# Optimization experiments

Measured on AMD Instinct MI355X. Metric: run time of the kernel, lower is better.

Reference implementation:

```python
import jax, jax.numpy as jnp
import numpy as np

N = 50000
E = 800000
D_IN = 128
HID = 128
LAT = 64
NEG_SLOPE = 0.2


def setup_inputs() -> dict:
    key = jax.random.key(0)
    ks = jax.random.split(key, 16)
    g = lambda k, shape: jax.random.normal(k, shape, dtype=jnp.float32) * (1.0 / np.sqrt(shape[0]))
    x = jax.random.normal(ks[0], (N, D_IN), dtype=jnp.float32)
    edge_index = jax.random.randint(ks[1], (2, E), 0, N, dtype=jnp.int64)
    return {
        "x": x,
        "edge_index": edge_index,
        # lin1: Linear(D_IN, HID)
        "lin1_w": g(ks[2], (D_IN, HID)),
        "lin1_b": jnp.zeros((HID,), jnp.float32),
        # conv1: GATConv((D_IN, D_IN) -> HID), heads=1
        "w1_src": g(ks[3], (D_IN, HID)),
        "w1_dst": g(ks[4], (D_IN, HID)),
        "a1_src": g(ks[5], (HID,)),
        "a1_dst": g(ks[6], (HID,)),
        "b1": jnp.zeros((HID,), jnp.float32),
        # conv2: GATConv((HID, HID) -> LAT), heads=1
        "w2_src": g(ks[7], (HID, LAT)),
        "w2_dst": g(ks[8], (HID, LAT)),
        "a2_src": g(ks[9], (LAT,)),
        "a2_dst": g(ks[10], (LAT,)),
        "b2": jnp.zeros((LAT,), jnp.float32),
    }


def _gat_conv(x, src, dst, w_src, w_dst, a_src, a_dst, b):
    """PyG GATConv, heads=1, add_self_loops=False. x: [N, Din]."""
    n = x.shape[0]
    hs = x @ w_src                    # [N, C] messages (source transform)
    hd = x @ w_dst                    # [N, C] destination transform
    alpha_s = hs @ a_src              # [N]
    alpha_d = hd @ a_dst              # [N]
    e = jax.nn.leaky_relu(alpha_s[src] + alpha_d[dst], NEG_SLOPE)  # [E]
    # segment softmax over incoming edges per destination node
    m = jax.ops.segment_max(e, dst, num_segments=n)
    ex = jnp.exp(e - m[dst])
    denom = jax.ops.segment_sum(ex, dst, num_segments=n)
    alpha = ex / (denom[dst] + 1e-16)                              # [E]
    msg = hs[src] * alpha[:, None]                                 # [E, C]
    out = jax.ops.segment_sum(msg, dst, num_segments=n)            # [N, C]
    return out + b


def reference(x, edge_index, lin1_w, lin1_b, w1_src, w1_dst, a1_src, a1_dst, b1,
              w2_src, w2_dst, a2_src, a2_dst, b2):
    src, dst = edge_index[0], edge_index[1]
    z = _gat_conv(x, src, dst, w1_src, w1_dst, a1_src, a1_dst, b1)
    z = jax.nn.relu(z + x @ lin1_w + lin1_b)
    z = _gat_conv(z, src, dst, w2_src, w2_dst, a2_src, a2_dst, b2)
    return z
```

## Files before the change

kernel.cpp:

```cpp
#include <hip/hip_runtime.h>

static constexpr int N_NODES = 50000;
static constexpr int N_EDGES = 800000;
static constexpr int NPART = 8;
static constexpr int PART_SZ = N_NODES / NPART;
static constexpr int NTILES = N_NODES / 16;

typedef __attribute__((ext_vector_type(8))) short bf16x8;
typedef __attribute__((ext_vector_type(4))) float f32x4;

__device__ __forceinline__ float bf2f(unsigned short u) {
  union { unsigned int i; float f; } v; v.i = ((unsigned int)u) << 16; return v.f;
}
__device__ __forceinline__ unsigned short f2bf(float f) {
  union { unsigned int i; float f; } v; v.f = f;
  unsigned int r = (v.i + 0x7fffu + ((v.i >> 16) & 1u)) >> 16;
  return (unsigned short)r;
}
__device__ __forceinline__ int clampN(int v) {
  unsigned u = (unsigned)v; return (u < (unsigned)N_NODES) ? (int)u : 0;
}

__global__ void k_zero_out(float* __restrict__ out, int n) {
  int i = blockIdx.x * 256 + threadIdx.x;
  if (i < n) out[i] = 0.f;
}

__global__ void k_zero_da(int* __restrict__ deg, float* __restrict__ as1) {
  int i = blockIdx.x * 256 + threadIdx.x;
  if (i < N_NODES) { deg[i] = 0; as1[i] = 0.f; }
}

__global__ void k_compact(const int* __restrict__ ei,
                          int* __restrict__ s32, int* __restrict__ d32) {
  int e = blockIdx.x * 256 + threadIdx.x;
  if (e < N_EDGES) {
    int z = ei[1] | ei[3] | ei[5] | ei[7];
    int f = (z == 0) ? 1 : 0;
    s32[e] = clampN(ei[(size_t)e << f]);
    d32[e] = clampN(ei[(size_t)(N_EDGES + e) << f]);
  }
}

__global__ void k_prepw(const float* __restrict__ w1_src, const float* __restrict__ wlin,
                        const float* __restrict__ w2_src,
                        const float* __restrict__ w1_dst, const float* __restrict__ a1_dst,
                        const float* __restrict__ w2_dst, const float* __restrict__ a2_dst,
                        unsigned short* __restrict__ w1T, unsigned short* __restrict__ w2T,
                        float* __restrict__ c1dst, float* __restrict__ c2dst) {
  int idx = blockIdx.x * 256 + threadIdx.x;
  if (idx < 256 * 128) {
    int c = idx >> 7, k = idx & 127;
    float v = (c < 128) ? w1_src[k * 128 + c] : wlin[k * 128 + (c - 128)];
    w1T[idx] = f2bf(v);
  } else if (idx < 256 * 128 + 64 * 128) {
    int r = idx - 256 * 128;
    int c = r >> 7, k = r & 127;
    w2T[r] = f2bf(w2_src[k * 64 + c]);
  } else if (blockIdx.x == 160) {
    int k = threadIdx.x;
    if (k < 128) {
      float s1 = 0.f;
      for (int c = 0; c < 128; ++c) s1 += w1_dst[k * 128 + c] * a1_dst[c];
      c1dst[k] = s1;
      float s2 = 0.f;
      for (int c = 0; c < 64; ++c) s2 += w2_dst[k * 64 + c] * a2_dst[c];
      c2dst[k] = s2;
    }
  }
}

__global__ __launch_bounds__(256) void k_prepx(
    const float* __restrict__ x, const float* __restrict__ c1dst,
    unsigned short* __restrict__ xb, float* __restrict__ ad1) {
  int gid = blockIdx.x * 256 + threadIdx.x;
  int row = gid >> 4, sl = gid & 15;
  const float* p = x + (size_t)row * 128 + sl * 8;
  float4 a0 = *(const float4*)p;
  float4 a1 = *(const float4*)(p + 4);
  uint4 o;
  o.x = (unsigned)f2bf(a0.x) | ((unsigned)f2bf(a0.y) << 16);
  o.y = (unsigned)f2bf(a0.z) | ((unsigned)f2bf(a0.w) << 16);
  o.z = (unsigned)f2bf(a1.x) | ((unsigned)f2bf(a1.y) << 16);
  o.w = (unsigned)f2bf(a1.z) | ((unsigned)f2bf(a1.w) << 16);
  *(uint4*)(xb + (size_t)row * 128 + sl * 8) = o;
  float4 ca = *(const float4*)(c1dst + sl * 8);
  float4 cb = *(const float4*)(c1dst + sl * 8 + 4);
  float sd = a0.x * ca.x + a0.y * ca.y + a0.z * ca.z + a0.w * ca.w +
             a1.x * cb.x + a1.y * cb.y + a1.z * cb.z + a1.w * cb.w;
  sd += __shfl_xor(sd, 1, 64);
  sd += __shfl_xor(sd, 2, 64);
  sd += __shfl_xor(sd, 4, 64);
  sd += __shfl_xor(sd, 8, 64);
  if (sl == 0) ad1[row] = sd;
}

__global__ __launch_bounds__(256) void k_gemm1(
    const unsigned short* __restrict__ xb, const unsigned short* __restrict__ w1T,
    const float* __restrict__ lin_b, const float* __restrict__ a1_src,
    unsigned short* __restrict__ hs1, unsigned short* __restrict__ linzb,
    float* __restrict__ as1) {
  int tid = threadIdx.x;
  int wv = tid >> 6, l = tid & 63;
  int lrow = l & 15, lk = l >> 4;
  int cb = wv * 64;
  bf16x8 wfrag[4][4];
#pragma unroll
  for (int ct = 0; ct < 4; ++ct)
#pragma unroll
    for (int ks = 0; ks < 4; ++ks)
      wfrag[ct][ks] = *(const bf16x8*)(w1T + (size_t)(cb + ct * 16 + lrow) * 128 + ks * 32 + lk * 8);
  for (int t = blockIdx.x; t < NTILES; t += gridDim.x) {
    int row = t * 16 + lrow;
    bf16x8 xfrag[4];
#pragma unroll
    for (int ks = 0; ks < 4; ++ks)
      xfrag[ks] = *(const bf16x8*)(xb + (size_t)row * 128 + ks * 32 + lk * 8);
    f32x4 acc[4] = {{0.f,0.f,0.f,0.f},{0.f,0.f,0.f,0.f},{0.f,0.f,0.f,0.f},{0.f,0.f,0.f,0.f}};
#pragma unroll
    for (int ks = 0; ks < 4; ++ks)
#pragma unroll
      for (int ct = 0; ct < 4; ++ct)
        acc[ct] = __builtin_amdgcn_mfma_f32_16x16x32_bf16(wfrag[ct][ks], xfrag[ks], acc[ct], 0, 0, 0);
    if (cb < 128) {
      float pa = 0.f;
#pragma unroll
      for (int ct = 0; ct < 4; ++ct) {
        int col0 = cb + ct * 16 + lk * 4;
        float4 av = *(const float4*)(a1_src + col0);
        pa += acc[ct][0] * av.x + acc[ct][1] * av.y + acc[ct][2] * av.z + acc[ct][3] * av.w;
        uint2 pv;
        pv.x = (unsigned)f2bf(acc[ct][0]) | ((unsigned)f2bf(acc[ct][1]) << 16);
        pv.y = (unsigned)f2bf(acc[ct][2]) | ((unsigned)f2bf(acc[ct][3]) << 16);
        *(uint2*)(hs1 + (size_t)row * 128 + col0) = pv;
      }
      pa += __shfl_xor(pa, 16, 64);
      pa += __shfl_xor(pa, 32, 64);
      if (l < 16) atomicAdd(&as1[t * 16 + l], pa);
    } else {
#pragma unroll
      for (int ct = 0; ct < 4; ++ct) {
        int col0 = cb - 128 + ct * 16 + lk * 4;
        float4 bv = *(const float4*)(lin_b + col0);
        uint2 pv;
        pv.x = (unsigned)f2bf(acc[ct][0] + bv.x) | ((unsigned)f2bf(acc[ct][1] + bv.y) << 16);
        pv.y = (unsigned)f2bf(acc[ct][2] + bv.z) | ((unsigned)f2bf(acc[ct][3] + bv.w) << 16);
        *(uint2*)(linzb + (size_t)row * 128 + col0) = pv;
      }
    }
  }
}

__global__ __launch_bounds__(256) void k_gemm2(
    const unsigned short* __restrict__ zb, const unsigned short* __restrict__ w2T,
    const float* __restrict__ a2_src, const float* __restrict__ c2dst,
    unsigned short* __restrict__ hs2, float* __restrict__ as2, float* __restrict__ ad2) {
  int tid = threadIdx.x;
  int wv = tid >> 6, l = tid & 63;
  int lrow = l & 15, lk = l >> 4;
  int g = blockIdx.x * 4 + wv;
  if (g >= NTILES) return;
  bf16x8 wfrag[4][4];
#pragma unroll
  for (int ct = 0; ct < 4; ++ct)
#pragma unroll
    for (int ks = 0; ks < 4; ++ks)
      wfrag[ct][ks] = *(const bf16x8*)(w2T + (size_t)(ct * 16 + lrow) * 128 + ks * 32 + lk * 8);
  int row = g * 16 + lrow;
  bf16x8 xfrag[4];
  float sd = 0.f;
#pragma unroll
  for (int ks = 0; ks < 4; ++ks) {
    bf16x8 af = *(const bf16x8*)(zb + (size_t)row * 128 + ks * 32 + lk * 8);
    xfrag[ks] = af;
    int k0 = ks * 32 + lk * 8;
    float4 ca = *(const float4*)(c2dst + k0);
    float4 cb = *(const float4*)(c2dst + k0 + 4);
    sd += bf2f((unsigned short)af[0]) * ca.x + bf2f((unsigned short)af[1]) * ca.y +
          bf2f((unsigned short)af[2]) * ca.z + bf2f((unsigned short)af[3]) * ca.w +
          bf2f((unsigned short)af[4]) * cb.x + bf2f((unsigned short)af[5]) * cb.y +
          bf2f((unsigned short)af[6]) * cb.z + bf2f((unsigned short)af[7]) * cb.w;
  }
  sd += __shfl_xor(sd, 16, 64);
  sd += __shfl_xor(sd, 32, 64);
  if (lk == 0) ad2[row] = sd;

  f32x4 acc[4] = {{0.f,0.f,0.f,0.f},{0.f,0.f,0.f,0.f},{0.f,0.f,0.f,0.f},{0.f,0.f,0.f,0.f}};
#pragma unroll
  for (int ks = 0; ks < 4; ++ks)
#pragma unroll
    for (int ct = 0; ct < 4; ++ct)
      acc[ct] = __builtin_amdgcn_mfma_f32_16x16x32_bf16(wfrag[ct][ks], xfrag[ks], acc[ct], 0, 0, 0);
  float pa = 0.f;
#pragma unroll
  for (int ct = 0; ct < 4; ++ct) {
    int col0 = ct * 16 + lk * 4;
    float4 av = *(const float4*)(a2_src + col0);
    pa += acc[ct][0] * av.x + acc[ct][1] * av.y + acc[ct][2] * av.z + acc[ct][3] * av.w;
    uint2 pv;
    pv.x = (unsigned)f2bf(acc[ct][0]) | ((unsigned)f2bf(acc[ct][1]) << 16);
    pv.y = (unsigned)f2bf(acc[ct][2]) | ((unsigned)f2bf(acc[ct][3]) << 16);
    *(uint2*)(hs2 + (size_t)row * 64 + col0) = pv;
  }
  pa += __shfl_xor(pa, 16, 64);
  pa += __shfl_xor(pa, 32, 64);
  if (lk == 0) as2[row] = pa;
}

__global__ void k_count(const int* __restrict__ d32, int* __restrict__ deg) {
  int part = blockIdx.x & (NPART - 1);
  int e = (blockIdx.x >> 3) * 256 + threadIdx.x;
  if (e < N_EDGES) {
    int d = d32[e];
    int lo = part * PART_SZ;
    if (d >= lo && d < lo + PART_SZ) atomicAdd(&deg[d], 1);
  }
}

__global__ __launch_bounds__(256) void k_scan1(const int* __restrict__ deg,
                                               int* __restrict__ offs,
                                               int* __restrict__ bsums, int n) {
  __shared__ int wsum[4];
  int i = blockIdx.x * 256 + threadIdx.x;
  int lane = threadIdx.x & 63, wid = threadIdx.x >> 6;
  int v = (i < n) ? deg[i] : 0;
  int s = v;
#pragma unroll
  for (int o = 1; o < 64; o <<= 1) { int t = __shfl_up(s, o, 64); if (lane >= o) s += t; }
  if (lane == 63) wsum[wid] = s;
  __syncthreads();
  if (threadIdx.x == 0) {
    int a = 0;
#pragma unroll
    for (int w = 0; w < 4; ++w) { a += wsum[w]; wsum[w] = a; }
  }
  __syncthreads();
  int base = (wid > 0) ? wsum[wid - 1] : 0;
  if (i < n) offs[i] = base + s - v;
  if (threadIdx.x == 0) bsums[blockIdx.x] = wsum[3];
}

__global__ __launch_bounds__(256) void k_scan2(int* __restrict__ bsums, int nb,
                                               int* __restrict__ offs, int n, int etot) {
  __shared__ int wsum[4];
  int tid = threadIdx.x, lane = tid & 63, wid = tid >> 6;
  int v = (tid < nb) ? bsums[tid] : 0;
  int s = v;
#pragma unroll
  for (int o = 1; o < 64; o <<= 1) { int t = __shfl_up(s, o, 64); if (lane >= o) s += t; }
  if (lane == 63) wsum[wid] = s;
  __syncthreads();
  if (tid == 0) {
    int a = 0;
#pragma unroll
    for (int w = 0; w < 4; ++w) { a += wsum[w]; wsum[w] = a; }
  }
  __syncthreads();
  int base = (wid > 0) ? wsum[wid - 1] : 0;
  if (tid < nb) bsums[tid] = base + s - v;
  if (tid == 0) offs[n] = etot;
}

__global__ __launch_bounds__(256) void k_scan3(int* __restrict__ offs, int* __restrict__ cursor,
                                               const int* __restrict__ bsums, int n) {
  int i = blockIdx.x * 256 + threadIdx.x;
  if (i < n) {
    int o = offs[i] + bsums[blockIdx.x];
    offs[i] = o;
    cursor[i] = o;
  }
}

__global__ void k_fill(const int* __restrict__ s32, const int* __restrict__ d32,
                       int* __restrict__ cursor, int* __restrict__ ssrc) {
  int part = blockIdx.x & (NPART - 1);
  int e = (blockIdx.x >> 3) * 256 + threadIdx.x;
  if (e < N_EDGES) {
    int d = d32[e];
    int lo = part * PART_SZ;
    if (d >= lo && d < lo + PART_SZ) {
      int p = atomicAdd(&cursor[d], 1);
      if ((unsigned)p < (unsigned)N_EDGES) ssrc[p] = s32[e];
    }
  }
}

__global__ __launch_bounds__(256) void k_agg1(
    const int* __restrict__ offs, const int* __restrict__ ssrc,
    const float* __restrict__ as_, const float* __restrict__ ad_,
    const unsigned short* __restrict__ hs1, const float* __restrict__ b1,
    unsigned short* __restrict__ linzb) {
  int node = (int)((blockIdx.x * 256 + threadIdx.x) >> 6);
  if (node >= N_NODES) return;
  int lane = threadIdx.x & 63;
  int g = lane >> 4, cl = lane & 15;
  int o0 = offs[node], o1 = offs[node + 1];
  if (!((unsigned)o0 <= (unsigned)N_EDGES && (unsigned)o1 <= (unsigned)N_EDGES && o0 <= o1))
    { o0 = 0; o1 = 0; }
  int deg = o1 - o0;
  float ad = ad_[node];
  float acc[8];
#pragma unroll
  for (int k = 0; k < 8; ++k) acc[k] = 0.f;
  float ssum = 0.f;
  for (int j = g; j < deg; j += 4) {
    int s = clampN(ssrc[o0 + j]);
    float e = as_[s] + ad;
    e = e > 0.f ? e : 0.2f * e;
    float w = __expf(e);
    uint4 hv = *(const uint4*)(hs1 + (size_t)s * 128 + cl * 8);
    ssum += w;
    acc[0] += w * __uint_as_float(hv.x << 16);
    acc[1] += w * __uint_as_float(hv.x & 0xffff0000u);
    acc[2] += w * __uint_as_float(hv.y << 16);
    acc[3] += w * __uint_as_float(hv.y & 0xffff0000u);
    acc[4] += w * __uint_as_float(hv.z << 16);
    acc[5] += w * __uint_as_float(hv.z & 0xffff0000u);
    acc[6] += w * __uint_as_float(hv.w << 16);
    acc[7] += w * __uint_as_float(hv.w & 0xffff0000u);
  }
  ssum += __shfl_xor(ssum, 16, 64);
  ssum += __shfl_xor(ssum, 32, 64);
#pragma unroll
  for (int k = 0; k < 8; ++k) {
    acc[k] += __shfl_xor(acc[k], 16, 64);
    acc[k] += __shfl_xor(acc[k], 32, 64);
  }
  if (g == 0) {
    float inv = 1.f / (ssum + 1e-16f);
    uint4 lv = *(const uint4*)(linzb + (size_t)node * 128 + cl * 8);
    float4 ba = *(const float4*)(b1 + cl * 8);
    float4 bb = *(const float4*)(b1 + cl * 8 + 4);
    float z[8];
    z[0] = acc[0] * inv + ba.x + __uint_as_float(lv.x << 16);
    z[1] = acc[1] * inv + ba.y + __uint_as_float(lv.x & 0xffff0000u);
    z[2] = acc[2] * inv + ba.z + __uint_as_float(lv.y << 16);
    z[3] = acc[3] * inv + ba.w + __uint_as_float(lv.y & 0xffff0000u);
    z[4] = acc[4] * inv + bb.x + __uint_as_float(lv.z << 16);
    z[5] = acc[5] * inv + bb.y + __uint_as_float(lv.z & 0xffff0000u);
    z[6] = acc[6] * inv + bb.z + __uint_as_float(lv.w << 16);
    z[7] = acc[7] * inv + bb.w + __uint_as_float(lv.w & 0xffff0000u);
#pragma unroll
    for (int k = 0; k < 8; ++k) z[k] = z[k] > 0.f ? z[k] : 0.f;
    uint4 ov;
    ov.x = (unsigned)f2bf(z[0]) | ((unsigned)f2bf(z[1]) << 16);
    ov.y = (unsigned)f2bf(z[2]) | ((unsigned)f2bf(z[3]) << 16);
    ov.z = (unsigned)f2bf(z[4]) | ((unsigned)f2bf(z[5]) << 16);
    ov.w = (unsigned)f2bf(z[6]) | ((unsigned)f2bf(z[7]) << 16);
    *(uint4*)(linzb + (size_t)node * 128 + cl * 8) = ov;
  }
}

__global__ __launch_bounds__(256) void k_agg2(
    const int* __restrict__ offs, const int* __restrict__ ssrc,
    const float* __restrict__ as_, const float* __restrict__ ad_,
    const unsigned short* __restrict__ hs2, const float* __restrict__ b2,
    float* __restrict__ out) {
  int node = (int)((blockIdx.x * 256 + threadIdx.x) >> 6);
  if (node >= N_NODES) return;
  int lane = threadIdx.x & 63;
  int g = lane >> 3, cl = lane & 7;
  int o0 = offs[node], o1 = offs[node + 1];
  if (!((unsigned)o0 <= (unsigned)N_EDGES && (unsigned)o1 <= (unsigned)N_EDGES && o0 <= o1))
    { o0 = 0; o1 = 0; }
  int deg = o1 - o0;
  float ad = ad_[node];
  float acc[8];
#pragma unroll
  for (int k = 0; k < 8; ++k) acc[k] = 0.f;
  float ssum = 0.f;
  for (int j = g; j < deg; j += 8) {
    int s = clampN(ssrc[o0 + j]);
    float e = as_[s] + ad;
    e = e > 0.f ? e : 0.2f * e;
    float w = __expf(e);
    uint4 hv = *(const uint4*)(hs2 + (size_t)s * 64 + cl * 8);
    ssum += w;
    acc[0] += w * __uint_as_float(hv.x << 16);
    acc[1] += w * __uint_as_float(hv.x & 0xffff0000u);
    acc[2] += w * __uint_as_float(hv.y << 16);
    acc[3] += w * __uint_as_float(hv.y & 0xffff0000u);
    acc[4] += w * __uint_as_float(hv.z << 16);
    acc[5] += w * __uint_as_float(hv.z & 0xffff0000u);
    acc[6] += w * __uint_as_float(hv.w << 16);
    acc[7] += w * __uint_as_float(hv.w & 0xffff0000u);
  }
  ssum += __shfl_xor(ssum, 8, 64);
  ssum += __shfl_xor(ssum, 16, 64);
  ssum += __shfl_xor(ssum, 32, 64);
#pragma unroll
  for (int k = 0; k < 8; ++k) {
    acc[k] += __shfl_xor(acc[k], 8, 64);
    acc[k] += __shfl_xor(acc[k], 16, 64);
    acc[k] += __shfl_xor(acc[k], 32, 64);
  }
  if (g == 0) {
    float inv = 1.f / (ssum + 1e-16f);
    float4 ba = *(const float4*)(b2 + cl * 8);
    float4 bb = *(const float4*)(b2 + cl * 8 + 4);
    float4 oa, ob;
    oa.x = acc[0] * inv + ba.x;
    oa.y = acc[1] * inv + ba.y;
    oa.z = acc[2] * inv + ba.z;
    oa.w = acc[3] * inv + ba.w;
    ob.x = acc[4] * inv + bb.x;
    ob.y = acc[5] * inv + bb.y;
    ob.z = acc[6] * inv + bb.z;
    ob.w = acc[7] * inv + bb.w;
    *(float4*)(out + (size_t)node * 64 + cl * 8) = oa;
    *(float4*)(out + (size_t)node * 64 + cl * 8 + 4) = ob;
  }
}

extern "C" void kernel_launch(void* const* d_in, const int* in_sizes, int n_in,
                              void* d_out, int out_size, void* d_ws, size_t ws_size,
                              hipStream_t stream) {
  (void)in_sizes; (void)n_in;
  const float* x      = (const float*)d_in[0];
  const int*   ei     = (const int*)d_in[1];
  const float* lin1_w = (const float*)d_in[2];
  const float* lin1_b = (const float*)d_in[3];
  const float* w1_src = (const float*)d_in[4];
  const float* w1_dst = (const float*)d_in[5];
  const float* a1_src = (const float*)d_in[6];
  const float* a1_dst = (const float*)d_in[7];
  const float* b1     = (const float*)d_in[8];
  const float* w2_src = (const float*)d_in[9];
  const float* w2_dst = (const float*)d_in[10];
  const float* a2_src = (const float*)d_in[11];
  const float* a2_dst = (const float*)d_in[12];
  const float* b2     = (const float*)d_in[13];
  float* out = (float*)d_out;

  char* ws = (char*)d_ws;
  size_t off = 0;
  auto alloc = [&](size_t bytes) -> void* {
    void* p = ws + off;
    off += (bytes + 255) & ~(size_t)255;
    return p;
  };
  float* c1dst = (float*)alloc(128 * 4);
  float* c2dst = (float*)alloc(128 * 4);
  unsigned short* w1T = (unsigned short*)alloc(256 * 128 * 2);
  unsigned short* w2T = (unsigned short*)alloc(64 * 128 * 2);
  int* deg     = (int*)alloc((size_t)N_NODES * 4);
  float* as1   = (float*)alloc((size_t)N_NODES * 4);
  int* offs    = (int*)alloc((size_t)(N_NODES + 1) * 4);
  int* cursor  = (int*)alloc((size_t)N_NODES * 4);
  int* bsums   = (int*)alloc(1024);
  float* ad1   = (float*)alloc((size_t)N_NODES * 4);
  int* s32     = (int*)alloc((size_t)N_EDGES * 4);
  int* d32     = (int*)alloc((size_t)N_EDGES * 4);
  unsigned short* hs1   = (unsigned short*)alloc((size_t)N_NODES * 128 * 2);
  unsigned short* linzb = (unsigned short*)alloc((size_t)N_NODES * 128 * 2);
  char* U = (char*)alloc((size_t)N_NODES * 128 * 2);
  unsigned short* xb  = (unsigned short*)U;
  int* ssrc           = (int*)U;
  unsigned short* hs2 = (unsigned short*)(U + (size_t)N_EDGES * 4);
  float* as2          = (float*)(U + (size_t)N_EDGES * 4 + (size_t)N_NODES * 128);
  float* ad2          = (float*)(U + (size_t)N_EDGES * 4 + (size_t)N_NODES * 128 + (size_t)N_NODES * 4);

  if (off > ws_size) {
    k_zero_out<<<(out_size + 255) / 256, 256, 0, stream>>>(out, out_size);
    return;
  }

  int ebl  = (N_EDGES + 255) / 256;
  int ebl8 = NPART * ebl;
  int nbl  = (N_NODES + 3) / 4;
  int nb   = (N_NODES + 255) / 256;
  k_zero_da<<<nb, 256, 0, stream>>>(deg, as1);
  k_prepw<<<161, 256, 0, stream>>>(w1_src, lin1_w, w2_src, w1_dst, a1_dst, w2_dst, a2_dst,
                                   w1T, w2T, c1dst, c2dst);
  k_compact<<<ebl, 256, 0, stream>>>(ei, s32, d32);
  k_prepx<<<NTILES, 256, 0, stream>>>(x, c1dst, xb, ad1);
  k_gemm1<<<1024, 256, 0, stream>>>(xb, w1T, lin1_b, a1_src, hs1, linzb, as1);
  k_count<<<ebl8, 256, 0, stream>>>(d32, deg);
  k_scan1<<<nb, 256, 0, stream>>>(deg, offs, bsums, N_NODES);
  k_scan2<<<1, 256, 0, stream>>>(bsums, nb, offs, N_NODES, N_EDGES);
  k_scan3<<<nb, 256, 0, stream>>>(offs, cursor, bsums, N_NODES);
  k_fill<<<ebl8, 256, 0, stream>>>(s32, d32, cursor, ssrc);
  k_agg1<<<nbl, 256, 0, stream>>>(offs, ssrc, as1, ad1, hs1, b1, linzb);
  k_gemm2<<<(NTILES + 3) / 4, 256, 0, stream>>>(linzb, w2T, a2_src, c2dst, hs2, as2, ad2);
  k_agg2<<<nbl, 256, 0, stream>>>(offs, ssrc, as2, ad2, hs2, b2, out);
}
```

Before: 206.1 us.

## Merge setup kernels into one launch and software-prefetch gathers in aggregation loops

Three small setup kernels (zeroing, edge index compaction, weight prep) are combined into one block-partitioned kernel, saving two launches. Both aggregation kernels now software-pipeline the neighbour gather: the next neighbour's attention scalar and feature row are loaded while the current one is accumulated, and the source index is read two iterations ahead. This aims to hide gather latency, at the cost of more registers and some extra out-of-range loads (index 0) at the end of each node's edge list.

```diff
diff --git a/kernel.cpp b/kernel.cpp
--- a/kernel.cpp
+++ b/kernel.cpp
@@ -26,47 +26,48 @@
   if (i < n) out[i] = 0.f;
 }
 
-__global__ void k_zero_da(int* __restrict__ deg, float* __restrict__ as1) {
-  int i = blockIdx.x * 256 + threadIdx.x;
-  if (i < N_NODES) { deg[i] = 0; as1[i] = 0.f; }
-}
-
-__global__ void k_compact(const int* __restrict__ ei,
-                          int* __restrict__ s32, int* __restrict__ d32) {
-  int e = blockIdx.x * 256 + threadIdx.x;
-  if (e < N_EDGES) {
-    int z = ei[1] | ei[3] | ei[5] | ei[7];
-    int f = (z == 0) ? 1 : 0;
-    s32[e] = clampN(ei[(size_t)e << f]);
-    d32[e] = clampN(ei[(size_t)(N_EDGES + e) << f]);
-  }
-}
-
-__global__ void k_prepw(const float* __restrict__ w1_src, const float* __restrict__ wlin,
+__global__ void k_setup(const int* __restrict__ ei,
+                        int* __restrict__ s32, int* __restrict__ d32,
+                        const float* __restrict__ w1_src, const float* __restrict__ wlin,
                         const float* __restrict__ w2_src,
                         const float* __restrict__ w1_dst, const float* __restrict__ a1_dst,
                         const float* __restrict__ w2_dst, const float* __restrict__ a2_dst,
                         unsigned short* __restrict__ w1T, unsigned short* __restrict__ w2T,
-                        float* __restrict__ c1dst, float* __restrict__ c2dst) {
-  int idx = blockIdx.x * 256 + threadIdx.x;
-  if (idx < 256 * 128) {
-    int c = idx >> 7, k = idx & 127;
-    float v = (c < 128) ? w1_src[k * 128 + c] : wlin[k * 128 + (c - 128)];
-    w1T[idx] = f2bf(v);
-  } else if (idx < 256 * 128 + 64 * 128) {
-    int r = idx - 256 * 128;
-    int c = r >> 7, k = r & 127;
-    w2T[r] = f2bf(w2_src[k * 64 + c]);
-  } else if (blockIdx.x == 160) {
-    int k = threadIdx.x;
-    if (k < 128) {
-      float s1 = 0.f;
-      for (int c = 0; c < 128; ++c) s1 += w1_dst[k * 128 + c] * a1_dst[c];
-      c1dst[k] = s1;
-      float s2 = 0.f;
-      for (int c = 0; c < 64; ++c) s2 += w2_dst[k * 64 + c] * a2_dst[c];
-      c2dst[k] = s2;
+                        float* __restrict__ c1dst, float* __restrict__ c2dst,
+                        int* __restrict__ deg, float* __restrict__ as1) {
+  int b = blockIdx.x;
+  if (b < 3125) {
+    int e = b * 256 + threadIdx.x;
+    if (e < N_EDGES) {
+      int z = ei[1] | ei[3] | ei[5] | ei[7];
+      int f = (z == 0) ? 1 : 0;
+      s32[e] = clampN(ei[(size_t)e << f]);
+      d32[e] = clampN(ei[(size_t)(N_EDGES + e) << f]);
     }
+  } else if (b < 3286) {
+    int idx = (b - 3125) * 256 + threadIdx.x;
+    if (idx < 256 * 128) {
+      int c = idx >> 7, k = idx & 127;
+      float v = (c < 128) ? w1_src[k * 128 + c] : wlin[k * 128 + (c - 128)];
+      w1T[idx] = f2bf(v);
+    } else if (idx < 256 * 128 + 64 * 128) {
+      int r = idx - 256 * 128;
+      int c = r >> 7, k = r & 127;
+      w2T[r] = f2bf(w2_src[k * 64 + c]);
+    } else if (b == 3285) {
+      int k = threadIdx.x;
+      if (k < 128) {
+        float s1 = 0.f;
+        for (int c = 0; c < 128; ++c) s1 += w1_dst[k * 128 + c] * a1_dst[c];
+        c1dst[k] = s1;
+        float s2 = 0.f;
+        for (int c = 0; c < 64; ++c) s2 += w2_dst[k * 64 + c] * a2_dst[c];
+        c2dst[k] = s2;
+      }
+    }
+  } else {
+    int i = (b - 3286) * 256 + threadIdx.x;
+    if (i < N_NODES) { deg[i] = 0; as1[i] = 0.f; }
   }
 }
 
@@ -303,21 +304,29 @@
 #pragma unroll
   for (int k = 0; k < 8; ++k) acc[k] = 0.f;
   float ssum = 0.f;
+  int s_nx = (g + 4 < deg) ? clampN(ssrc[o0 + g + 4]) : 0;
+  int s_cu = (g < deg) ? clampN(ssrc[o0 + g]) : 0;
+  float as_cu = as_[s_cu];
+  uint4 hv_cu = *(const uint4*)(hs1 + (size_t)s_cu * 128 + cl * 8);
   for (int j = g; j < deg; j += 4) {
-    int s = clampN(ssrc[o0 + j]);
-    float e = as_[s] + ad;
+    int s_n2 = (j + 8 < deg) ? clampN(ssrc[o0 + j + 8]) : 0;
+    float as_nx = as_[s_nx];
+    uint4 hv_nx = *(const uint4*)(hs1 + (size_t)s_nx * 128 + cl * 8);
+    float e = as_cu + ad;
     e = e > 0.f ? e : 0.2f * e;
     float w = __expf(e);
-    uint4 hv = *(const uint4*)(hs1 + (size_t)s * 128 + cl * 8);
     ssum += w;
-    acc[0] += w * __uint_as_float(hv.x << 16);
-    acc[1] += w * __uint_as_float(hv.x & 0xffff0000u);
-    acc[2] += w * __uint_as_float(hv.y << 16);
-    acc[3] += w * __uint_as_float(hv.y & 0xffff0000u);
-    acc[4] += w * __uint_as_float(hv.z << 16);
-    acc[5] += w * __uint_as_float(hv.z & 0xffff0000u);
-    acc[6] += w * __uint_as_float(hv.w << 16);
-    acc[7] += w * __uint_as_float(hv.w & 0xffff0000u);
+    acc[0] += w * __uint_as_float(hv_cu.x << 16);
+    acc[1] += w * __uint_as_float(hv_cu.x & 0xffff0000u);
+    acc[2] += w * __uint_as_float(hv_cu.y << 16);
+    acc[3] += w * __uint_as_float(hv_cu.y & 0xffff0000u);
+    acc[4] += w * __uint_as_float(hv_cu.z << 16);
+    acc[5] += w * __uint_as_float(hv_cu.z & 0xffff0000u);
+    acc[6] += w * __uint_as_float(hv_cu.w << 16);
+    acc[7] += w * __uint_as_float(hv_cu.w & 0xffff0000u);
+    s_nx = s_n2;
+    as_cu = as_nx;
+    hv_cu = hv_nx;
   }
   ssum += __shfl_xor(ssum, 16, 64);
   ssum += __shfl_xor(ssum, 32, 64);
@@ -369,21 +378,29 @@
 #pragma unroll
   for (int k = 0; k < 8; ++k) acc[k] = 0.f;
   float ssum = 0.f;
+  int s_nx = (g + 8 < deg) ? clampN(ssrc[o0 + g + 8]) : 0;
+  int s_cu = (g < deg) ? clampN(ssrc[o0 + g]) : 0;
+  float as_cu = as_[s_cu];
+  uint4 hv_cu = *(const uint4*)(hs2 + (size_t)s_cu * 64 + cl * 8);
   for (int j = g; j < deg; j += 8) {
-    int s = clampN(ssrc[o0 + j]);
-    float e = as_[s] + ad;
+    int s_n2 = (j + 16 < deg) ? clampN(ssrc[o0 + j + 16]) : 0;
+    float as_nx = as_[s_nx];
+    uint4 hv_nx = *(const uint4*)(hs2 + (size_t)s_nx * 64 + cl * 8);
+    float e = as_cu + ad;
     e = e > 0.f ? e : 0.2f * e;
     float w = __expf(e);
-    uint4 hv = *(const uint4*)(hs2 + (size_t)s * 64 + cl * 8);
     ssum += w;
-    acc[0] += w * __uint_as_float(hv.x << 16);
-    acc[1] += w * __uint_as_float(hv.x & 0xffff0000u);
-    acc[2] += w * __uint_as_float(hv.y << 16);
-    acc[3] += w * __uint_as_float(hv.y & 0xffff0000u);
-    acc[4] += w * __uint_as_float(hv.z << 16);
-    acc[5] += w * __uint_as_float(hv.z & 0xffff0000u);
-    acc[6] += w * __uint_as_float(hv.w << 16);
-    acc[7] += w * __uint_as_float(hv.w & 0xffff0000u);
+    acc[0] += w * __uint_as_float(hv_cu.x << 16);
+    acc[1] += w * __uint_as_float(hv_cu.x & 0xffff0000u);
+    acc[2] += w * __uint_as_float(hv_cu.y << 16);
+    acc[3] += w * __uint_as_float(hv_cu.y & 0xffff0000u);
+    acc[4] += w * __uint_as_float(hv_cu.z << 16);
+    acc[5] += w * __uint_as_float(hv_cu.z & 0xffff0000u);
+    acc[6] += w * __uint_as_float(hv_cu.w << 16);
+    acc[7] += w * __uint_as_float(hv_cu.w & 0xffff0000u);
+    s_nx = s_n2;
+    as_cu = as_nx;
+    hv_cu = hv_nx;
   }
   ssum += __shfl_xor(ssum, 8, 64);
   ssum += __shfl_xor(ssum, 16, 64);
@@ -465,14 +482,12 @@
     return;
   }
 
-  int ebl  = (N_EDGES + 255) / 256;
-  int ebl8 = NPART * ebl;
+  int ebl8 = NPART * ((N_EDGES + 255) / 256);
   int nbl  = (N_NODES + 3) / 4;
   int nb   = (N_NODES + 255) / 256;
-  k_zero_da<<<nb, 256, 0, stream>>>(deg, as1);
-  k_prepw<<<161, 256, 0, stream>>>(w1_src, lin1_w, w2_src, w1_dst, a1_dst, w2_dst, a2_dst,
-                                   w1T, w2T, c1dst, c2dst);
-  k_compact<<<ebl, 256, 0, stream>>>(ei, s32, d32);
+  k_setup<<<3482, 256, 0, stream>>>(ei, s32, d32, w1_src, lin1_w, w2_src,
+                                    w1_dst, a1_dst, w2_dst, a2_dst,
+                                    w1T, w2T, c1dst, c2dst, deg, as1);
   k_prepx<<<NTILES, 256, 0, stream>>>(x, c1dst, xb, ad1);
   k_gemm1<<<1024, 256, 0, stream>>>(xb, w1T, lin1_b, a1_src, hs1, linzb, as1);
   k_count<<<ebl8, 256, 0, stream>>>(d32, deg);
```

Result: faster. 195.9 us (median of 2 runs) (-4.9%).
